# Optimization experiments

Hardware: AMD Instinct MI355X
Metric: run time of the kernel (lower is better)

## Reference

```python
import jax, jax.numpy as jnp
import numpy as np

N = 40000      # nodes
E = 640000     # edges
IN_C = 128
HID = 256
OUT_C = 10
G = 64         # graphs in batch


def setup_inputs() -> dict:
    key = jax.random.key(0)
    ks = jax.random.split(key, 8)
    x = jax.random.normal(ks[0], (N, IN_C), dtype=jnp.float32)
    edge_index = jax.random.randint(ks[1], (2, E), 0, N, dtype=jnp.int64)
    batch = jnp.sort(jax.random.randint(ks[2], (N,), 0, G, dtype=jnp.int64))
    W1 = jax.random.normal(ks[3], (IN_C, HID), dtype=jnp.float32) / np.sqrt(IN_C)
    b1 = jnp.zeros((HID,), dtype=jnp.float32)
    W2 = jax.random.normal(ks[4], (HID, HID), dtype=jnp.float32) / np.sqrt(HID)
    b2 = jnp.zeros((HID,), dtype=jnp.float32)
    Wlin = jax.random.normal(ks[5], (HID, OUT_C), dtype=jnp.float32) / np.sqrt(HID)
    blin = jnp.zeros((OUT_C,), dtype=jnp.float32)
    return {"x": x, "edge_index": edge_index, "batch": batch,
            "W1": W1, "b1": b1, "W2": W2, "b2": b2, "Wlin": Wlin, "blin": blin}


def _gcn_conv(x, W, b, src, dst, n_nodes):
    # PyG GCNConv: linear transform, self-loop-augmented sym normalization, scatter-add, bias
    h = x @ W                                   # [N, F]
    deg = jnp.zeros((n_nodes,), h.dtype).at[dst].add(1.0)  # in-degree incl. self loops
    dis = jax.lax.rsqrt(jnp.maximum(deg, 1.0))             # deg >= 1 due to self loops
    norm = dis[src] * dis[dst]                  # [E+N]
    msg = h[src] * norm[:, None]                # gather + scale
    out = jnp.zeros((n_nodes, h.shape[1]), h.dtype).at[dst].add(msg)
    return out + b


def reference(x, edge_index, batch, W1, b1, W2, b2, Wlin, blin):
    n = x.shape[0]
    loop = jnp.arange(n, dtype=edge_index.dtype)
    src = jnp.concatenate([edge_index[0], loop])  # add self loops (PyG default)
    dst = jnp.concatenate([edge_index[1], loop])

    h = jax.nn.relu(_gcn_conv(x, W1, b1, src, dst, n))
    h = jax.nn.relu(_gcn_conv(h, W2, b2, src, dst, n))

    # global_mean_pool over graph ids
    sums = jax.ops.segment_sum(h, batch, num_segments=G)            # [G, HID]
    cnts = jax.ops.segment_sum(jnp.ones((n,), h.dtype), batch, num_segments=G)
    pooled = sums / jnp.maximum(cnts, 1.0)[:, None]

    return pooled @ Wlin + blin                  # [G, OUT_C]
```

## Files before the change

kernel.cpp:

```cpp
#include <hip/hip_runtime.h>

#define NN    40000
#define EE    640000
#define INC   128
#define HID   256
#define OUTC  10
#define GG    64
#define CAP   64

typedef unsigned short u16;
typedef __attribute__((ext_vector_type(8))) short short8;
typedef __attribute__((ext_vector_type(4))) float f32x4;

__device__ __forceinline__ float bf2f(u16 h) {
    return __uint_as_float(((unsigned)h) << 16);
}
__device__ __forceinline__ u16 f2bf(float f) {
    unsigned u = __float_as_uint(f);
    unsigned r = u + 0x7FFFu + ((u >> 16) & 1u);
    return (u16)(r >> 16);
}

__device__ __forceinline__ void gload_lds16(const u16* g, u16* l) {
    __builtin_amdgcn_global_load_lds(
        (const __attribute__((address_space(1))) unsigned int*)g,
        (__attribute__((address_space(3))) unsigned int*)l,
        16, 0, 0);
}

#define WTOT (INC * HID + HID * HID)
__global__ void build_kernel(const int* __restrict__ src, const int* __restrict__ dst,
                             int* __restrict__ cnt, u16* __restrict__ col, int e4,
                             const float* __restrict__ W1, u16* __restrict__ w1h,
                             const float* __restrict__ W2, u16* __restrict__ w2h,
                             const float* __restrict__ x, u16* __restrict__ xq,
                             int total4) {
    int i = blockIdx.x * blockDim.x + threadIdx.x;
    if (i < e4) {
        int4 d = ((const int4*)dst)[i];
        int4 s = ((const int4*)src)[i];
        int r0 = atomicAdd(&cnt[d.x], 1);
        int r1 = atomicAdd(&cnt[d.y], 1);
        int r2 = atomicAdd(&cnt[d.z], 1);
        int r3 = atomicAdd(&cnt[d.w], 1);
        if (r0 < CAP) col[(d.x << 6) + r0] = (u16)s.x;
        if (r1 < CAP) col[(d.y << 6) + r1] = (u16)s.y;
        if (r2 < CAP) col[(d.z << 6) + r2] = (u16)s.z;
        if (r3 < CAP) col[(d.w << 6) + r3] = (u16)s.w;
    } else if (i < e4 + WTOT) {
        int idx = i - e4;
        const float* W; u16* Th; int K;
        if (idx < INC * HID) { W = W1; Th = w1h; K = INC; }
        else { W = W2; Th = w2h; K = HID; idx -= INC * HID; }
        int k = idx >> 8;
        int n = idx & 255;
        Th[(size_t)n * K + k] = f2bf(W[idx]);
    } else {
        int j = i - e4 - WTOT;
        if (j < total4) {
            float4 v = ((const float4*)x)[j];
            ushort4 o;
            o.x = f2bf(v.x); o.y = f2bf(v.y);
            o.z = f2bf(v.z); o.w = f2bf(v.w);
            ((ushort4*)xq)[j] = o;
        }
    }
}

#define BM 128
#define BN 128
#define BK 64
#define PGL 8

template<int MODE>
__global__ __launch_bounds__(256) void mgemm_kernel(
    const u16* __restrict__ A,
    const u16* __restrict__ Bh,
    const float* __restrict__ bias,
    const int* __restrict__ cnt,
    u16* __restrict__ Cout,
    const int* __restrict__ batch, float* __restrict__ pooled,
    int M, int K)
{
    __shared__ __align__(16) u16 As [BM * BK];
    __shared__ __align__(16) u16 Bhs[BN * BK];
    __shared__ float ptile[MODE == 1 ? PGL * BN : 1];

    const int tid  = threadIdx.x;
    const int lane = tid & 63;
    const int wave = tid >> 6;
    const int ln   = lane & 15;
    const int qd   = lane >> 4;
    const int wm   = (wave & 1) * 64;
    const int wn   = (wave >> 1) * 64;
    const int m0   = blockIdx.x * BM;
    const int n0   = blockIdx.y * BN;

    f32x4 acc[4][4];
#pragma unroll
    for (int i = 0; i < 4; ++i)
#pragma unroll
        for (int j = 0; j < 4; ++j) acc[i][j] = (f32x4)(0.0f);

    if (MODE == 1) {
        for (int t = tid; t < PGL * BN; t += 256) ptile[t] = 0.0f;
    }

    const int rl = lane >> 3;
    const int su = lane & 7;

    for (int k0 = 0; k0 < K; k0 += BK) {
#pragma unroll
        for (int L = 0; L < 4; ++L) {
            int rloc = (wave * 4 + L) * 8 + rl;
            int sv   = (su ^ (rloc & 7)) * 8;
            int ga   = m0 + rloc; if (ga >= M) ga = M - 1;
            gload_lds16(A  + (size_t)ga * K          + k0 + sv, As  + (size_t)(wave * 4 + L) * 512);
            gload_lds16(Bh + (size_t)(n0 + rloc) * K + k0 + sv, Bhs + (size_t)(wave * 4 + L) * 512);
        }
        __syncthreads();

#pragma unroll
        for (int ks = 0; ks < 2; ++ks) {
            const int fsw = ((ks * 4 + qd) ^ (ln & 7)) * 8;
            short8 af[4], bfh[4];
#pragma unroll
            for (int t = 0; t < 4; ++t) {
                af[t]  = *(const short8*)(As  + (wm + t * 16 + ln) * BK + fsw);
                bfh[t] = *(const short8*)(Bhs + (wn + t * 16 + ln) * BK + fsw);
            }
#pragma unroll
            for (int ti = 0; ti < 4; ++ti)
#pragma unroll
                for (int tj = 0; tj < 4; ++tj)
                    acc[ti][tj] = __builtin_amdgcn_mfma_f32_16x16x32_bf16(
                        af[ti], bfh[tj], acc[ti][tj], 0, 0, 0);
        }
        __syncthreads();
    }

    float bcol[4];
#pragma unroll
    for (int tj = 0; tj < 4; ++tj) bcol[tj] = bias[n0 + wn + tj * 16 + ln];

    if (MODE == 0) {
#pragma unroll
        for (int ti = 0; ti < 4; ++ti) {
#pragma unroll
            for (int r = 0; r < 4; ++r) {
                int row = m0 + wm + ti * 16 + qd * 4 + r;
                if (row < M) {
                    float dm = rsqrtf((float)(cnt[row] + 1));
                    u16* crow = Cout + (size_t)row * HID;
#pragma unroll
                    for (int tj = 0; tj < 4; ++tj) {
                        float v = fmaxf(acc[ti][tj][r] + bcol[tj], 0.0f);
                        crow[n0 + wn + tj * 16 + ln] = f2bf(v * dm);
                    }
                }
            }
        }
    } else {
        int bg[16];
#pragma unroll
        for (int ti = 0; ti < 4; ++ti)
#pragma unroll
            for (int r = 0; r < 4; ++r) {
                int row = m0 + wm + ti * 16 + qd * 4 + r;
                bg[ti * 4 + r] = (row < M) ? batch[row] : -1;
            }
        const int g_lo = batch[m0];
        const int g_hi = batch[min(m0 + BM, M) - 1];
        for (int g = g_lo; g <= g_hi; ++g) {
            float cs[4] = {0.0f, 0.0f, 0.0f, 0.0f};
#pragma unroll
            for (int ti = 0; ti < 4; ++ti)
#pragma unroll
                for (int r = 0; r < 4; ++r)
                    if (bg[ti * 4 + r] == g) {
#pragma unroll
                        for (int tj = 0; tj < 4; ++tj)
                            cs[tj] += fmaxf(acc[ti][tj][r] + bcol[tj], 0.0f);
                    }
#pragma unroll
            for (int tj = 0; tj < 4; ++tj) {
                cs[tj] += __shfl_xor(cs[tj], 16);
                cs[tj] += __shfl_xor(cs[tj], 32);
            }
            if (qd == 0) {
                int gl = g - g_lo;
#pragma unroll
                for (int tj = 0; tj < 4; ++tj) {
                    int c = wn + tj * 16 + ln;
                    if (gl < PGL) atomicAdd(&ptile[gl * BN + c], cs[tj]);
                    else atomicAdd(&pooled[(size_t)g * HID + n0 + c], cs[tj]);
                }
            }
        }
        __syncthreads();
        const int g0 = batch[m0];
        for (int t = tid; t < PGL * BN; t += 256) {
            float v = ptile[t];
            if (v != 0.0f) {
                int gl = t / BN, c = t % BN;
                atomicAdd(&pooled[(size_t)(g0 + gl) * HID + n0 + c], v);
            }
        }
    }
}

template<int F, bool PERDIS>
__global__ __launch_bounds__(256) void agg_kernel(
    const u16* __restrict__ hs, const int* __restrict__ cnt,
    const u16* __restrict__ col, u16* __restrict__ out, int n_nodes)
{
    constexpr int L  = F / 8;
    constexpr int G  = 64 / L;
    constexpr int UF = 16 / G;
    const int lane = threadIdx.x & 63;
    const int n    = (blockIdx.x * blockDim.x + threadIdx.x) >> 6;
    if (n >= n_nodes) return;
    const int li = lane % L;
    const int gi = lane / L;

    const int base0 = n << 6;
    const int total = 1 + cnt[n];

    float acc[8];
#pragma unroll
    for (int i = 0; i < 8; ++i) acc[i] = 0.0f;

    for (int base = 0; base < total; base += G * UF) {
        int  idxs[UF];
        bool valid[UF];
#pragma unroll
        for (int u = 0; u < UF; ++u) {
            int it = base + u * G + gi;
            valid[u] = (it < total);
            idxs[u] = 0;
            if (valid[u]) idxs[u] = (it == 0) ? n : (int)col[base0 + it - 1];
        }
        uint4 w[UF];
        int   cv[UF];
#pragma unroll
        for (int u = 0; u < UF; ++u)
            if (valid[u]) {
                w[u] = *(const uint4*)(hs + (size_t)idxs[u] * F + li * 8);
                if (PERDIS) cv[u] = cnt[idxs[u]];
            }
#pragma unroll
        for (int u = 0; u < UF; ++u)
            if (valid[u]) {
                float d = PERDIS ? rsqrtf((float)(cv[u] + 1)) : 1.0f;
                unsigned uu[4] = {w[u].x, w[u].y, w[u].z, w[u].w};
#pragma unroll
                for (int q = 0; q < 4; ++q) {
                    if (PERDIS) {
                        acc[2 * q]     = fmaf(d, __uint_as_float(uu[q] << 16), acc[2 * q]);
                        acc[2 * q + 1] = fmaf(d, __uint_as_float(uu[q] & 0xFFFF0000u), acc[2 * q + 1]);
                    } else {
                        acc[2 * q]     += __uint_as_float(uu[q] << 16);
                        acc[2 * q + 1] += __uint_as_float(uu[q] & 0xFFFF0000u);
                    }
                }
            }
    }

#pragma unroll
    for (int off = 32; off >= L; off >>= 1)
#pragma unroll
        for (int i = 0; i < 8; ++i)
            acc[i] += __shfl_xor(acc[i], off);

    if (gi == 0) {
        float d = rsqrtf((float)total);
        unsigned r[4];
#pragma unroll
        for (int q = 0; q < 4; ++q) {
            unsigned l16 = (unsigned)f2bf(acc[2 * q] * d);
            unsigned h16 = (unsigned)f2bf(acc[2 * q + 1] * d);
            r[q] = l16 | (h16 << 16);
        }
        *(uint4*)(out + (size_t)n * F + li * 8) = make_uint4(r[0], r[1], r[2], r[3]);
    }
}

__global__ __launch_bounds__(256) void pool_finalize_kernel(
    const float* __restrict__ pooled, const int* __restrict__ batch,
    const float* __restrict__ Wlin, const float* __restrict__ blin,
    float* __restrict__ out, int n_nodes)
{
    const int g = blockIdx.x;
    const int j = threadIdx.x;
    int lo = 0, hi = n_nodes;
    while (lo < hi) { int mid = (lo + hi) >> 1; if (batch[mid] < g) lo = mid + 1; else hi = mid; }
    const int start = lo;
    lo = start; hi = n_nodes;
    while (lo < hi) { int mid = (lo + hi) >> 1; if (batch[mid] < g + 1) lo = mid + 1; else hi = mid; }
    const int cnt = lo - start;

    float pv = pooled[(size_t)g * HID + j] / fmaxf((float)cnt, 1.0f);

    __shared__ float pl[HID];
    pl[j] = pv;
    __syncthreads();
    if (j < OUTC) {
        float o = blin[j];
        for (int k = 0; k < HID; ++k) o = fmaf(pl[k], Wlin[k * OUTC + j], o);
        out[g * OUTC + j] = o;
    }
}

extern "C" void kernel_launch(void* const* d_in, const int* in_sizes, int n_in,
                              void* d_out, int out_size, void* d_ws, size_t ws_size,
                              hipStream_t stream) {
    const float* x     = (const float*)d_in[0];
    const int*   ei    = (const int*)  d_in[1];
    const int*   batch = (const int*)  d_in[2];
    const float* W1    = (const float*)d_in[3];
    const float* b1    = (const float*)d_in[4];
    const float* W2    = (const float*)d_in[5];
    const float* b2    = (const float*)d_in[6];
    const float* Wlin  = (const float*)d_in[7];
    const float* blin  = (const float*)d_in[8];
    float* out = (float*)d_out;

    const int* src = ei;
    const int* dst = ei + EE;

    char* p = (char*)d_ws;
    u16*   xq  = (u16*)p;   p += (size_t)NN * INC * sizeof(u16);
    u16*   xab = (u16*)p;   p += (size_t)NN * INC * sizeof(u16);
    u16*   h1s = (u16*)p;   p += (size_t)NN * HID * sizeof(u16);
    u16*   a2b = (u16*)p;   p += (size_t)NN * HID * sizeof(u16);
    u16*   w1h = (u16*)p;   p += (size_t)HID * INC * sizeof(u16);
    u16*   w2h = (u16*)p;   p += (size_t)HID * HID * sizeof(u16);
    char* zbase = p;
    float* pooled = (float*)p; p += (size_t)GG * HID * sizeof(float);
    int* cnt    = (int*)p;  p += (size_t)NN * sizeof(int);
    size_t zbytes = (size_t)(p - zbase);
    u16* col    = (u16*)p;  p += (size_t)NN * CAP * sizeof(u16);
    (void)ws_size; (void)n_in; (void)in_sizes; (void)out_size;

    const int TB = 256;
    const int e4     = EE / 4;
    const int total4 = NN * INC / 4;
    const int build_threads = e4 + WTOT + total4;
    const int nb_build = (build_threads + TB - 1) / TB;

    hipMemsetAsync(zbase, 0, zbytes, stream);
    build_kernel<<<nb_build, TB, 0, stream>>>(src, dst, cnt, col, e4,
                                              W1, w1h, W2, w2h, x, xq, total4);

    dim3 ggrid((NN + BM - 1) / BM, HID / BN);
    const int agg_blocks = (NN * 64 + TB - 1) / TB;

    agg_kernel<INC, true><<<agg_blocks, TB, 0, stream>>>(xq, cnt, col, xab, NN);
    mgemm_kernel<0><<<ggrid, 256, 0, stream>>>(xab, w1h, b1, cnt, h1s,
                                               batch, pooled, NN, INC);

    agg_kernel<HID, false><<<agg_blocks, TB, 0, stream>>>(h1s, cnt, col, a2b, NN);
    mgemm_kernel<1><<<ggrid, 256, 0, stream>>>(a2b, w2h, b2, cnt, (u16*)nullptr,
                                               batch, pooled, NN, HID);

    pool_finalize_kernel<<<GG, 256, 0, stream>>>(pooled, batch, Wlin, blin, out, NN);
}
```

Before: 232.1 us.

## Fuse memset, build and first aggregation into one cooperative grid-synced kernel

```diff
diff --git a/kernel.cpp b/kernel.cpp
--- a/kernel.cpp
+++ b/kernel.cpp
@@ -1,4 +1,6 @@
 #include <hip/hip_runtime.h>
+#include <hip/hip_cooperative_groups.h>
+namespace cg = cooperative_groups;
 
 #define NN    40000
 #define EE    640000
@@ -29,13 +31,15 @@
 }
 
 #define WTOT (INC * HID + HID * HID)
-__global__ void build_kernel(const int* __restrict__ src, const int* __restrict__ dst,
-                             int* __restrict__ cnt, u16* __restrict__ col, int e4,
-                             const float* __restrict__ W1, u16* __restrict__ w1h,
-                             const float* __restrict__ W2, u16* __restrict__ w2h,
-                             const float* __restrict__ x, u16* __restrict__ xq,
-                             int total4) {
-    int i = blockIdx.x * blockDim.x + threadIdx.x;
+__device__ __forceinline__ void build_item(
+    int i, int e4, int total4,
+    const int* __restrict__ src, const int* __restrict__ dst,
+    int* __restrict__ cnt, u16* __restrict__ col,
+    const float* __restrict__ W1, u16* __restrict__ w1h,
+    const float* __restrict__ W2, u16* __restrict__ w2h,
+    const float* __restrict__ x, u16* __restrict__ xq,
+    const int* __restrict__ batch, int* __restrict__ gseg)
+{
     if (i < e4) {
         int4 d = ((const int4*)dst)[i];
         int4 s = ((const int4*)src)[i];
@@ -55,16 +59,128 @@
         int k = idx >> 8;
         int n = idx & 255;
         Th[(size_t)n * K + k] = f2bf(W[idx]);
+    } else if (i < e4 + WTOT + total4) {
+        int j = i - e4 - WTOT;
+        float4 v = ((const float4*)x)[j];
+        ushort4 o;
+        o.x = f2bf(v.x); o.y = f2bf(v.y);
+        o.z = f2bf(v.z); o.w = f2bf(v.w);
+        ((ushort4*)xq)[j] = o;
     } else {
-        int j = i - e4 - WTOT;
-        if (j < total4) {
-            float4 v = ((const float4*)x)[j];
-            ushort4 o;
-            o.x = f2bf(v.x); o.y = f2bf(v.y);
-            o.z = f2bf(v.z); o.w = f2bf(v.w);
-            ((ushort4*)xq)[j] = o;
-        }
-    }
+        int g = i - e4 - WTOT - total4;
+        if (g <= GG) {
+            int lo = 0, hi = NN;
+            while (lo < hi) { int mid = (lo + hi) >> 1; if (batch[mid] < g) lo = mid + 1; else hi = mid; }
+            gseg[g] = lo;
+        }
+    }
+}
+
+__global__ void build_kernel(const int* __restrict__ src, const int* __restrict__ dst,
+                             int* __restrict__ cnt, u16* __restrict__ col, int e4,
+                             const float* __restrict__ W1, u16* __restrict__ w1h,
+                             const float* __restrict__ W2, u16* __restrict__ w2h,
+                             const float* __restrict__ x, u16* __restrict__ xq,
+                             int total4, const int* __restrict__ batch,
+                             int* __restrict__ gseg) {
+    int i = blockIdx.x * blockDim.x + threadIdx.x;
+    build_item(i, e4, total4, src, dst, cnt, col, W1, w1h, W2, w2h, x, xq, batch, gseg);
+}
+
+__device__ __forceinline__ void agg1_node(
+    int n, int lane, const u16* __restrict__ xq, const int* __restrict__ cnt,
+    const u16* __restrict__ col, u16* __restrict__ out)
+{
+    constexpr int F  = INC;
+    constexpr int L  = F / 8;
+    constexpr int G  = 64 / L;
+    constexpr int UF = 16 / G;
+    const int li = lane % L;
+    const int gi = lane / L;
+
+    const int base0 = n << 6;
+    const int total = 1 + cnt[n];
+
+    float acc[8];
+#pragma unroll
+    for (int i = 0; i < 8; ++i) acc[i] = 0.0f;
+
+    for (int base = 0; base < total; base += G * UF) {
+        int  idxs[UF];
+        bool valid[UF];
+#pragma unroll
+        for (int u = 0; u < UF; ++u) {
+            int it = base + u * G + gi;
+            valid[u] = (it < total);
+            idxs[u] = 0;
+            if (valid[u]) idxs[u] = (it == 0) ? n : (int)col[base0 + it - 1];
+        }
+        uint4 w[UF];
+        int   cv[UF];
+#pragma unroll
+        for (int u = 0; u < UF; ++u)
+            if (valid[u]) {
+                w[u] = *(const uint4*)(xq + (size_t)idxs[u] * F + li * 8);
+                cv[u] = cnt[idxs[u]];
+            }
+#pragma unroll
+        for (int u = 0; u < UF; ++u)
+            if (valid[u]) {
+                float d = rsqrtf((float)(cv[u] + 1));
+                unsigned uu[4] = {w[u].x, w[u].y, w[u].z, w[u].w};
+#pragma unroll
+                for (int q = 0; q < 4; ++q) {
+                    acc[2 * q]     = fmaf(d, __uint_as_float(uu[q] << 16), acc[2 * q]);
+                    acc[2 * q + 1] = fmaf(d, __uint_as_float(uu[q] & 0xFFFF0000u), acc[2 * q + 1]);
+                }
+            }
+    }
+
+#pragma unroll
+    for (int off = 32; off >= L; off >>= 1)
+#pragma unroll
+        for (int i = 0; i < 8; ++i)
+            acc[i] += __shfl_xor(acc[i], off);
+
+    if (gi == 0) {
+        float d = rsqrtf((float)total);
+        unsigned r[4];
+#pragma unroll
+        for (int q = 0; q < 4; ++q) {
+            unsigned l16 = (unsigned)f2bf(acc[2 * q] * d);
+            unsigned h16 = (unsigned)f2bf(acc[2 * q + 1] * d);
+            r[q] = l16 | (h16 << 16);
+        }
+        *(uint4*)(out + (size_t)n * F + li * 8) = make_uint4(r[0], r[1], r[2], r[3]);
+    }
+}
+
+__global__ __launch_bounds__(256) void fused_front_kernel(
+    const int* __restrict__ src, const int* __restrict__ dst,
+    int* __restrict__ cnt, u16* __restrict__ col, int e4,
+    const float* __restrict__ W1, u16* __restrict__ w1h,
+    const float* __restrict__ W2, u16* __restrict__ w2h,
+    const float* __restrict__ x, u16* __restrict__ xq, int total4,
+    int zwords, int* __restrict__ zbase,
+    const int* __restrict__ batch, int* __restrict__ gseg,
+    u16* __restrict__ xab)
+{
+    cg::grid_group grid = cg::this_grid();
+    const int gtid   = blockIdx.x * blockDim.x + threadIdx.x;
+    const int stride = gridDim.x * blockDim.x;
+
+    for (int i = gtid; i < zwords; i += stride) zbase[i] = 0;
+    grid.sync();
+
+    const int bt = e4 + WTOT + total4 + GG + 1;
+    for (int i = gtid; i < bt; i += stride)
+        build_item(i, e4, total4, src, dst, cnt, col, W1, w1h, W2, w2h, x, xq, batch, gseg);
+    grid.sync();
+
+    const int lane   = threadIdx.x & 63;
+    const int nwaves = stride >> 6;
+    for (int n = gtid >> 6; n < NN; n += nwaves)
+        agg1_node(n, lane, xq, cnt, col, xab);
 }
 
 #define BM 128
@@ -286,20 +402,15 @@
 }
 
 __global__ __launch_bounds__(256) void pool_finalize_kernel(
-    const float* __restrict__ pooled, const int* __restrict__ batch,
+    const float* __restrict__ pooled, const int* __restrict__ gseg,
     const float* __restrict__ Wlin, const float* __restrict__ blin,
-    float* __restrict__ out, int n_nodes)
+    float* __restrict__ out)
 {
     const int g = blockIdx.x;
     const int j = threadIdx.x;
-    int lo = 0, hi = n_nodes;
-    while (lo < hi) { int mid = (lo + hi) >> 1; if (batch[mid] < g) lo = mid + 1; else hi = mid; }
-    const int start = lo;
-    lo = start; hi = n_nodes;
-    while (lo < hi) { int mid = (lo + hi) >> 1; if (batch[mid] < g + 1) lo = mid + 1; else hi = mid; }
-    const int cnt = lo - start;
-
-    float pv = pooled[(size_t)g * HID + j] / fmaxf((float)cnt, 1.0f);
+    const int cntg = gseg[g + 1] - gseg[g];
+
+    float pv = pooled[(size_t)g * HID + j] / fmaxf((float)cntg, 1.0f);
 
     __shared__ float pl[HID];
     pl[j] = pv;
@@ -340,22 +451,48 @@
     int* cnt    = (int*)p;  p += (size_t)NN * sizeof(int);
     size_t zbytes = (size_t)(p - zbase);
     u16* col    = (u16*)p;  p += (size_t)NN * CAP * sizeof(u16);
+    int* gseg   = (int*)p;  p += (GG + 1) * sizeof(int);
     (void)ws_size; (void)n_in; (void)in_sizes; (void)out_size;
 
     const int TB = 256;
-    const int e4     = EE / 4;
-    const int total4 = NN * INC / 4;
-    const int build_threads = e4 + WTOT + total4;
-    const int nb_build = (build_threads + TB - 1) / TB;
-
-    hipMemsetAsync(zbase, 0, zbytes, stream);
-    build_kernel<<<nb_build, TB, 0, stream>>>(src, dst, cnt, col, e4,
-                                              W1, w1h, W2, w2h, x, xq, total4);
+    int e4v     = EE / 4;
+    int total4v = NN * INC / 4;
+    int zwords  = (int)(zbytes / 4);
+    int* zbi    = (int*)zbase;
+
+    bool coop_ok = false;
+    {
+        int maxb = 0;
+        hipError_t oe = hipOccupancyMaxActiveBlocksPerMultiprocessor(
+            &maxb, fused_front_kernel, TB, 0);
+        int fgrid = maxb * 256;
+        if (fgrid > 2048) fgrid = 2048;
+        if (oe == hipSuccess && fgrid >= 256) {
+            void* kargs[] = {
+                (void*)&src, (void*)&dst, (void*)&cnt, (void*)&col, (void*)&e4v,
+                (void*)&W1, (void*)&w1h, (void*)&W2, (void*)&w2h,
+                (void*)&x, (void*)&xq, (void*)&total4v,
+                (void*)&zwords, (void*)&zbi, (void*)&batch, (void*)&gseg,
+                (void*)&xab };
+            hipError_t le = hipLaunchCooperativeKernel(
+                fused_front_kernel, dim3(fgrid), dim3(TB), kargs, 0u, stream);
+            coop_ok = (le == hipSuccess);
+        }
+    }
+    if (!coop_ok) {
+        const int build_threads = e4v + WTOT + total4v + GG + 1;
+        const int nb_build = (build_threads + TB - 1) / TB;
+        const int agg_blocks = (NN * 64 + TB - 1) / TB;
+        hipMemsetAsync(zbase, 0, zbytes, stream);
+        build_kernel<<<nb_build, TB, 0, stream>>>(src, dst, cnt, col, e4v,
+                                                  W1, w1h, W2, w2h, x, xq,
+                                                  total4v, batch, gseg);
+        agg_kernel<INC, true><<<agg_blocks, TB, 0, stream>>>(xq, cnt, col, xab, NN);
+    }
 
     dim3 ggrid((NN + BM - 1) / BM, HID / BN);
     const int agg_blocks = (NN * 64 + TB - 1) / TB;
 
-    agg_kernel<INC, true><<<agg_blocks, TB, 0, stream>>>(xq, cnt, col, xab, NN);
     mgemm_kernel<0><<<ggrid, 256, 0, stream>>>(xab, w1h, b1, cnt, h1s,
                                                batch, pooled, NN, INC);
 
@@ -363,5 +500,5 @@
     mgemm_kernel<1><<<ggrid, 256, 0, stream>>>(a2b, w2h, b2, cnt, (u16*)nullptr,
                                                batch, pooled, NN, HID);
 
-    pool_finalize_kernel<<<GG, 256, 0, stream>>>(pooled, batch, Wlin, blin, out, NN);
-}
+    pool_finalize_kernel<<<GG, 256, 0, stream>>>(pooled, gseg, Wlin, blin, out);
+}
```

New measurement: 432.2 us. 1.86x slower.
